# Kernel optimization log

Measured on AMD Instinct MI355X. Metric: run time of the kernel, lower is better.

## Reference

```python
import jax, jax.numpy as jnp
import numpy as np

N = 100000
E = 1600000
IN_DIM = 128
HID = 16      # per-head dim
HEADS = 4
FEAT = HID * HEADS  # 64
OUT_DIM = 64
EPS = 0.5
LAYERS = 2


def setup_inputs() -> dict:
    key = jax.random.key(0)
    ks = jax.random.split(key, 8)
    return {
        "h": jax.random.normal(ks[0], (N, IN_DIM), dtype=jnp.float32),
        "src": jax.random.randint(ks[1], (E,), 0, N, dtype=jnp.int64),
        "dst": jax.random.randint(ks[2], (E,), 0, N, dtype=jnp.int64),
        "t1_W": jax.random.normal(ks[3], (IN_DIM, FEAT), dtype=jnp.float32) * 0.1,
        "t1_b": jnp.zeros((FEAT,), dtype=jnp.float32),
        "t2_W": jax.random.normal(ks[4], (FEAT, OUT_DIM), dtype=jnp.float32) * 0.1,
        "t2_b": jnp.zeros((OUT_DIM,), dtype=jnp.float32),
        "gate_W": jax.random.normal(ks[5], (LAYERS, 2 * HID, 1), dtype=jnp.float32) * 0.2,
        "gate_b": jnp.zeros((LAYERS, 1), dtype=jnp.float32),
    }


def reference(h, src, dst, t1_W, t1_b, t2_W, t2_b, gate_W, gate_b):
    # t1 + relu
    x = jax.nn.relu(h @ t1_W + t1_b)            # [N, FEAT]
    raw = x

    # symmetric degree norm: deg^-0.5 from in-degrees (clamped at 1)
    deg = jax.ops.segment_sum(jnp.ones((E,), x.dtype), dst, num_segments=N)
    norm = jnp.clip(deg, 1.0, None) ** -0.5     # [N]

    xh = x.reshape(N, HEADS, HID)
    edge_norm = norm[dst] * norm[src]           # [E]
    h1 = raw
    # NOTE: original forward never updates x inside the loop; each layer
    # consumes the same relu(t1(h)) and only the last layer's h0 survives.
    for l in range(LAYERS):
        hs = xh[src]                            # [E, H, D] gather src
        hd = xh[dst]                            # [E, H, D] gather dst
        hcat = jnp.concatenate([hd, hs], axis=-1)  # [E, H, 2D]
        s = jnp.tanh(hcat @ gate_W[l] + gate_b[l])[..., 0]  # [E, H]
        s = s * edge_norm[:, None]
        e_h = (hs * s[..., None]).reshape(E, FEAT)          # [E, FEAT]
        h0 = jax.ops.segment_sum(e_h, dst, num_segments=N)  # scatter-sum
        h1 = EPS * raw + h0

    return h1 @ t2_W + t2_b                      # [N, OUT_DIM]
```

## Files before the change

### kernel.cpp

```cpp
#include <hip/hip_runtime.h>
#include <hip/hip_fp16.h>
#include <math.h>

#define N_NODES 100000
#define E_EDGES 1600000
#define IN_DIM  128
#define FEAT    64
#define OUT_DIM 64
#define NBKT    391
#define CAP     6144
#define RNG     4096
#define NSCB    ((E_EDGES + RNG - 1) / RNG)
#define G1B2    ((N_NODES + 127) / 128)
#define HTS     130

typedef float vfloat2 __attribute__((ext_vector_type(2)));

__global__ __launch_bounds__(256) void k_binscatter(
    const int* __restrict__ src, const int* __restrict__ dst,
    int* __restrict__ bucket_cursor, int* __restrict__ binned)
{
    __shared__ int hist[NBKT];
    __shared__ int baseS[NBKT];
    __shared__ int cursor[NBKT];
    __shared__ int gbase[NBKT];
    __shared__ int sA[512], sB[512];
    __shared__ int buf[RNG];
    __shared__ unsigned short bkt[RNG];

    const int tid  = threadIdx.x;
    const int e0   = blockIdx.x * RNG;
    const int ecnt = min(RNG, E_EDGES - e0);

    for (int i = tid; i < NBKT; i += 256) hist[i] = 0;
    __syncthreads();

    int dsave[16];
#pragma unroll
    for (int k = 0; k < 16; ++k) {
        int e = e0 + k * 256 + tid;
        int d = (e < E_EDGES) ? dst[e] : -1;
        dsave[k] = d;
        if (d >= 0) atomicAdd(&hist[d >> 8], 1);
    }
    __syncthreads();

    for (int i = tid; i < 512; i += 256) sA[i] = (i < NBKT) ? hist[i] : 0;
    __syncthreads();
    int* pa = sA; int* pb = sB;
    for (int off = 1; off < 512; off <<= 1) {
        for (int i = tid; i < 512; i += 256)
            pb[i] = pa[i] + ((i >= off) ? pa[i - off] : 0);
        __syncthreads();
        int* t = pa; pa = pb; pb = t;
    }
    for (int i = tid; i < NBKT; i += 256) {
        int ex = pa[i] - hist[i];
        baseS[i]  = ex;
        cursor[i] = ex;
    }
    __syncthreads();

#pragma unroll
    for (int k = 0; k < 16; ++k) {
        int d = dsave[k];
        if (d >= 0) {
            int e   = e0 + k * 256 + tid;
            int s   = src[e];
            int b   = d >> 8;
            int pos = atomicAdd(&cursor[b], 1);
            buf[pos] = ((d & 255) << 17) | s;
            bkt[pos] = (unsigned short)b;
        }
    }
    __syncthreads();

    for (int t = tid; t < NBKT; t += 256) {
        int cnt = hist[t];
        int g   = cnt ? atomicAdd(&bucket_cursor[t], cnt) : 0;
        gbase[t] = g - baseS[t];
    }
    __syncthreads();

    for (int i = tid; i < ecnt; i += 256) {
        int b   = bkt[i];
        int off = gbase[b] + i;
        if (off < CAP) binned[b * CAP + off] = buf[i];
    }
}

__global__ __launch_bounds__(256) void k_bucketfinal(
    const int* __restrict__ binned, const int* __restrict__ bucket_cursor,
    int* __restrict__ deg, int* __restrict__ rowptr, int* __restrict__ src_sorted)
{
    __shared__ int sA[512], sB[512];
    __shared__ int hist[256];
    __shared__ int scn[256];
    __shared__ int cur[256];
    const int b   = blockIdx.x;
    const int tid = threadIdx.x;

    for (int i = tid; i < 512; i += 256) sA[i] = (i < NBKT) ? bucket_cursor[i] : 0;
    __syncthreads();
    int* pa = sA; int* pb = sB;
    for (int off = 1; off < 512; off <<= 1) {
        for (int i = tid; i < 512; i += 256)
            pb[i] = pa[i] + ((i >= off) ? pa[i - off] : 0);
        __syncthreads();
        int* t = pa; pa = pb; pb = t;
    }
    const int cnt  = bucket_cursor[b];
    const int eb   = pa[b] - cnt;
    const int base = b * CAP;
    __syncthreads();

    hist[tid] = 0;
    __syncthreads();
    for (int i = tid; i < cnt; i += 256)
        atomicAdd(&hist[binned[base + i] >> 17], 1);
    __syncthreads();

    int v = hist[tid];
    scn[tid] = v;
    __syncthreads();
    for (int off = 1; off < 256; off <<= 1) {
        int add = (tid >= off) ? scn[tid - off] : 0;
        __syncthreads();
        scn[tid] += add;
        __syncthreads();
    }
    int ex = scn[tid] - v;
    cur[tid] = ex;
    int n = b * 256 + tid;
    if (n < N_NODES) {
        deg[n]    = v;
        rowptr[n] = eb + ex;
    }
    if (b == 0 && tid == 0) rowptr[N_NODES] = E_EDGES;
    __syncthreads();

    for (int i = tid; i < cnt; i += 256) {
        int p   = binned[base + i];
        int dl  = p >> 17;
        int pos = atomicAdd(&cur[dl], 1);
        src_sorted[eb + pos] = p & 0x1FFFF;
    }
}

__global__ __launch_bounds__(256, 3) void k_gemm1(
    const float* __restrict__ h, const float* __restrict__ W1,
    const float* __restrict__ b1, const int* __restrict__ deg,
    const float* __restrict__ gate_W,
    __half* __restrict__ xs2h, unsigned int* __restrict__ xq,
    float* __restrict__ aproj, float* __restrict__ bproj)
{
    __shared__ float Ws[IN_DIM * FEAT];
    __shared__ float hT[16 * HTS];
    const int tid = threadIdx.x;
    const int r0  = blockIdx.x * 128;

    for (int i = tid; i < IN_DIM * FEAT / 4; i += 256)
        ((float4*)Ws)[i] = ((const float4*)W1)[i];

    const int rg = tid >> 2;
    const int cg = tid & 3;
    const int c0 = cg * 16;
    float acc[2][16];
#pragma unroll
    for (int i = 0; i < 2; ++i)
#pragma unroll
        for (int j = 0; j < 16; ++j) acc[i][j] = 0.f;

    for (int kc = 0; kc < IN_DIM / 16; ++kc) {
        float4 f[2];
#pragma unroll
        for (int it = 0; it < 2; ++it) {
            int idx = tid + it * 256;
            int row = idx >> 2;
            int q   = idx & 3;
            int gr  = r0 + row;
            f[it] = (gr < N_NODES)
                ? *(const float4*)(h + (size_t)gr * IN_DIM + kc * 16 + q * 4)
                : make_float4(0.f, 0.f, 0.f, 0.f);
        }
        __syncthreads();
#pragma unroll
        for (int it = 0; it < 2; ++it) {
            int idx = tid + it * 256;
            int row = idx >> 2;
            int q   = idx & 3;
            hT[(q * 4 + 0) * HTS + row] = f[it].x;
            hT[(q * 4 + 1) * HTS + row] = f[it].y;
            hT[(q * 4 + 2) * HTS + row] = f[it].z;
            hT[(q * 4 + 3) * HTS + row] = f[it].w;
        }
        __syncthreads();
#pragma unroll
        for (int kk = 0; kk < 16; ++kk) {
            float2 a2 = *(const float2*)&hT[kk * HTS + rg * 2];
            const float* wrow = &Ws[(kc * 16 + kk) * FEAT + c0];
            float4 w0 = ((const float4*)wrow)[0];
            float4 w1 = ((const float4*)wrow)[1];
            float4 w2 = ((const float4*)wrow)[2];
            float4 w3 = ((const float4*)wrow)[3];
            const float w[16] = {w0.x, w0.y, w0.z, w0.w, w1.x, w1.y, w1.z, w1.w,
                                 w2.x, w2.y, w2.z, w2.w, w3.x, w3.y, w3.z, w3.w};
#pragma unroll
            for (int j = 0; j < 16; ++j) {
                acc[0][j] = fmaf(a2.x, w[j], acc[0][j]);
                acc[1][j] = fmaf(a2.y, w[j], acc[1][j]);
            }
        }
    }

#pragma unroll
    for (int i = 0; i < 2; ++i) {
        int r = r0 + rg * 2 + i;
        if (r >= N_NODES) continue;
        float nr = rsqrtf(fmaxf((float)deg[r], 1.f));
        float xa = 0.f, xb = 0.f;
        alignas(16) __half hv[16];
        float vs[16];
#pragma unroll
        for (int j = 0; j < 16; ++j) {
            float v = acc[i][j] + b1[c0 + j];
            v = v > 0.f ? v : 0.f;
            xa = fmaf(v, gate_W[32 + j], xa);
            xb = fmaf(v, gate_W[48 + j], xb);
            float sv = v * nr;
            vs[j] = sv;
            hv[j] = __float2half(sv);
        }
        float4* xp = (float4*)(xs2h + (size_t)r * FEAT + c0);
        xp[0] = *(const float4*)&hv[0];
        xp[1] = *(const float4*)&hv[8];
        unsigned int u[4];
#pragma unroll
        for (int q = 0; q < 4; ++q) {
            unsigned int t = 0;
            t = __builtin_amdgcn_cvt_pk_fp8_f32(vs[q*4+0], vs[q*4+1], t, false);
            t = __builtin_amdgcn_cvt_pk_fp8_f32(vs[q*4+2], vs[q*4+3], t, true);
            u[q] = t;
        }
        ((uint4*)xq)[(size_t)r * 4 + cg] = make_uint4(u[0], u[1], u[2], u[3]);
        aproj[(size_t)r * 4 + cg] = xa;
        bproj[(size_t)r * 4 + cg] = xb;
    }
}

__global__ __launch_bounds__(256) void k_aggregate(
    const uint4* __restrict__ xq4, const __half2* __restrict__ xs2h2,
    const float* __restrict__ aproj, const float* __restrict__ bproj,
    const int* __restrict__ rowptr, const int* __restrict__ src_sorted,
    const float* __restrict__ gate_b, float* __restrict__ v_out)
{
    const int tid    = threadIdx.x;
    const int lane   = tid & 63;
    const int e      = lane >> 2;
    const int l4     = lane & 3;
    const int wave   = blockIdx.x * 4 + (tid >> 6);
    const int nwaves = gridDim.x * 4;
    const float gb   = gate_b[1];
    const float C    = 2.8853900817779268f;

    for (int n = wave; n < N_NODES; n += nwaves) {
        const int beg = rowptr[n];
        const int end = rowptr[n + 1];
        const int cnt = end - beg;
        const float a_d = aproj[(size_t)n * 4 + l4] + gb;

        float acc[16];
#pragma unroll
        for (int k = 0; k < 16; ++k) acc[k] = 0.f;

        if (cnt > 0) {
            const int last = end - 1;
            int  j0  = beg + e;
            bool ok0 = j0 < end;
            int  s0  = src_sorted[ok0 ? j0 : last];
            uint4 x0 = xq4[(size_t)s0 * 4 + l4];
            float b0 = bproj[(size_t)s0 * 4 + l4];
            int  j1  = j0 + 16;
            bool ok1 = j1 < end;
            int  s1  = src_sorted[ok1 ? j1 : last];

            for (int j = beg; j < end; j += 16) {
                const bool more = (j + 16) < end;
                uint4 x1 = make_uint4(0u, 0u, 0u, 0u);
                float b1 = 0.f;
                int   s2 = s1;
                bool  ok2 = false;
                if (more) {
                    x1 = xq4[(size_t)s1 * 4 + l4];
                    b1 = bproj[(size_t)s1 * 4 + l4];
                    int j2 = j + 32 + e;
                    ok2 = j2 < end;
                    s2 = src_sorted[ok2 ? j2 : last];
                }
                float ex = __builtin_amdgcn_exp2f(C * (a_d + b0));
                float t  = 1.f - 2.f * __builtin_amdgcn_rcpf(ex + 1.f);
                t = ok0 ? t : 0.f;
#pragma unroll
                for (int w = 0; w < 4; ++w) {
                    const unsigned int xw = ((const unsigned int*)&x0)[w];
                    vfloat2 lo = __builtin_amdgcn_cvt_pk_f32_fp8(xw, false);
                    vfloat2 hi = __builtin_amdgcn_cvt_pk_f32_fp8(xw, true);
                    acc[w * 4 + 0] = fmaf(t, lo[0], acc[w * 4 + 0]);
                    acc[w * 4 + 1] = fmaf(t, lo[1], acc[w * 4 + 1]);
                    acc[w * 4 + 2] = fmaf(t, hi[0], acc[w * 4 + 2]);
                    acc[w * 4 + 3] = fmaf(t, hi[1], acc[w * 4 + 3]);
                }
                if (more) {
                    x0 = x1; b0 = b1; ok0 = ok1; ok1 = ok2; s1 = s2;
                }
            }
        }

        const bool elo = (e & 1) == 0;
        float r8[8];
#pragma unroll
        for (int i = 0; i < 8; ++i) {
            float give = elo ? acc[8 + i] : acc[i];
            float got  = __shfl_xor(give, 4, 64);
            r8[i] = (elo ? acc[i] : acc[8 + i]) + got;
        }
        const bool e2lo = (e & 2) == 0;
        float v4[4];
#pragma unroll
        for (int i = 0; i < 4; ++i) {
            float give = e2lo ? r8[4 + i] : r8[i];
            float got  = __shfl_xor(give, 8, 64);
            v4[i] = (e2lo ? r8[i] : r8[4 + i]) + got;
        }
#pragma unroll
        for (int i = 0; i < 4; ++i) v4[i] += __shfl_xor(v4[i], 16, 64);
#pragma unroll
        for (int i = 0; i < 4; ++i) v4[i] += __shfl_xor(v4[i], 32, 64);

        const float dg = fmaxf((float)cnt, 1.f);
        const float nd = rsqrtf(dg);
        const float sd = dg * nd;

        if (e < 4) {
            const int q = ((e & 1) << 1) | ((e >> 1) & 1);
            const int Q = l4 * 4 + q;
            const __half2* hp = xs2h2 + (size_t)n * 32 + Q * 2;
            float2 fa = __half22float2(hp[0]);
            float2 fb = __half22float2(hp[1]);
            float4 v;
            v.x = fmaf(0.5f * sd, fa.x, v4[0] * nd);
            v.y = fmaf(0.5f * sd, fa.y, v4[1] * nd);
            v.z = fmaf(0.5f * sd, fb.x, v4[2] * nd);
            v.w = fmaf(0.5f * sd, fb.y, v4[3] * nd);
            ((float4*)v_out)[(size_t)n * 16 + Q] = v;
        }
    }
}

__global__ __launch_bounds__(256) void k_gemm2(
    float* __restrict__ v, const float* __restrict__ W2, const float* __restrict__ b2)
{
    const int tid    = threadIdx.x;
    const int lane   = tid & 63;
    const int kc     = lane >> 4;
    const int oq     = lane & 15;
    const int wave   = blockIdx.x * 4 + (tid >> 6);
    const int nwaves = gridDim.x * 4;

    float4 wreg[16];
#pragma unroll
    for (int j = 0; j < 16; ++j)
        wreg[j] = *(const float4*)(W2 + (size_t)(kc * 16 + j) * OUT_DIM + oq * 4);
    const float4 bq = ((const float4*)b2)[oq];

    for (int n = wave; n < N_NODES; n += nwaves) {
        const float4* vrow = (const float4*)(v + (size_t)n * FEAT) + kc * 4;
        float4 q0 = vrow[0], q1 = vrow[1], q2 = vrow[2], q3 = vrow[3];
        const float vs[16] = {q0.x, q0.y, q0.z, q0.w, q1.x, q1.y, q1.z, q1.w,
                              q2.x, q2.y, q2.z, q2.w, q3.x, q3.y, q3.z, q3.w};
        float ax = 0.f, ay = 0.f, az = 0.f, aw = 0.f;
#pragma unroll
        for (int j = 0; j < 16; ++j) {
            ax = fmaf(vs[j], wreg[j].x, ax);
            ay = fmaf(vs[j], wreg[j].y, ay);
            az = fmaf(vs[j], wreg[j].z, az);
            aw = fmaf(vs[j], wreg[j].w, aw);
        }
        ax += __shfl_xor(ax, 16, 64); ay += __shfl_xor(ay, 16, 64);
        az += __shfl_xor(az, 16, 64); aw += __shfl_xor(aw, 16, 64);
        ax += __shfl_xor(ax, 32, 64); ay += __shfl_xor(ay, 32, 64);
        az += __shfl_xor(az, 32, 64); aw += __shfl_xor(aw, 32, 64);
        if (kc == 0) {
            float4 o = make_float4(ax + bq.x, ay + bq.y, az + bq.z, aw + bq.w);
            ((float4*)v)[(size_t)n * 16 + oq] = o;
        }
    }
}

extern "C" void kernel_launch(void* const* d_in, const int* in_sizes, int n_in,
                              void* d_out, int out_size, void* d_ws, size_t ws_size,
                              hipStream_t stream)
{
    const float* h   = (const float*)d_in[0];
    const int*   src = (const int*)d_in[1];
    const int*   dst = (const int*)d_in[2];
    const float* W1  = (const float*)d_in[3];
    const float* b1  = (const float*)d_in[4];
    const float* W2  = (const float*)d_in[5];
    const float* b2  = (const float*)d_in[6];
    const float* gW  = (const float*)d_in[7];
    const float* gb  = (const float*)d_in[8];
    float* out = (float*)d_out;

    int* bucket_cursor = (int*)d_ws;
    int* binned        = bucket_cursor + NBKT;
    int* src_sorted    = binned + (size_t)NBKT * CAP;
    int* rowptr        = src_sorted + E_EDGES;
    int* deg           = rowptr + (N_NODES + 1);
    float* aproj       = (float*)(deg + N_NODES);
    float* bproj       = aproj + (size_t)N_NODES * 4;
    __half* xs2h       = (__half*)(bproj + (size_t)N_NODES * 4);
    unsigned int* xq   = (unsigned int*)(xs2h + (size_t)N_NODES * FEAT);

    hipMemsetAsync(bucket_cursor, 0, NBKT * sizeof(int), stream);

    k_binscatter <<<NSCB, 256, 0, stream>>>(src, dst, bucket_cursor, binned);
    k_bucketfinal<<<NBKT, 256, 0, stream>>>(binned, bucket_cursor, deg, rowptr, src_sorted);
    k_gemm1      <<<G1B2, 256, 0, stream>>>(h, W1, b1, deg, gW, xs2h, xq, aproj, bproj);
    k_aggregate  <<<2048, 256, 0, stream>>>((const uint4*)xq, (const __half2*)xs2h,
                                            aproj, bproj, rowptr, src_sorted, gb, out);
    k_gemm2      <<<1024, 256, 0, stream>>>(out, W2, b2);
}
```

Measured before the change: 259.5 us.

## Use 256-row 512-thread blocks in gemm1 with register prefetch of next K-chunk

Each k_gemm1 block now covers 256 rows with 512 threads, so the 32KB W1 copy in shared memory is loaded half as often per row. The next 16-wide slice of h is prefetched into registers while the current slice is being multiplied, overlapping global loads with FMA work. The cost is larger blocks with less control over occupancy, since the min-blocks launch bound was dropped. Shared memory per block also grows with the wider transposed tile.

After: 308.1 us. +18.7%, slower.

```diff
diff --git a/kernel.cpp b/kernel.cpp
--- a/kernel.cpp
+++ b/kernel.cpp
@@ -11,8 +11,7 @@
 #define CAP     6144
 #define RNG     4096
 #define NSCB    ((E_EDGES + RNG - 1) / RNG)
-#define G1B2    ((N_NODES + 127) / 128)
-#define HTS     130
+#define G1B     ((N_NODES + 255) / 256)
 
 typedef float vfloat2 __attribute__((ext_vector_type(2)));
 
@@ -147,7 +146,7 @@
     }
 }
 
-__global__ __launch_bounds__(256, 3) void k_gemm1(
+__global__ __launch_bounds__(512) void k_gemm1(
     const float* __restrict__ h, const float* __restrict__ W1,
     const float* __restrict__ b1, const int* __restrict__ deg,
     const float* __restrict__ gate_W,
@@ -155,11 +154,11 @@
     float* __restrict__ aproj, float* __restrict__ bproj)
 {
     __shared__ float Ws[IN_DIM * FEAT];
-    __shared__ float hT[16 * HTS];
+    __shared__ float hT[16 * 260];
     const int tid = threadIdx.x;
-    const int r0  = blockIdx.x * 128;
-
-    for (int i = tid; i < IN_DIM * FEAT / 4; i += 256)
+    const int r0  = blockIdx.x * 256;
+
+    for (int i = tid; i < IN_DIM * FEAT / 4; i += 512)
         ((float4*)Ws)[i] = ((const float4*)W1)[i];
 
     const int rg = tid >> 2;
@@ -171,33 +170,37 @@
 #pragma unroll
         for (int j = 0; j < 16; ++j) acc[i][j] = 0.f;
 
+    const int qk    = tid & 3;
+    const int row0  = (tid >> 2);
+    const int grow0 = r0 + row0;
+    const int grow1 = r0 + row0 + 128;
+    const bool ok0r = grow0 < N_NODES;
+    const bool ok1r = grow1 < N_NODES;
+    const float* hp0 = h + (size_t)grow0 * IN_DIM + qk * 4;
+    const float* hp1 = h + (size_t)grow1 * IN_DIM + qk * 4;
+
+    float4 f[2];
+    f[0] = ok0r ? *(const float4*)hp0 : make_float4(0.f, 0.f, 0.f, 0.f);
+    f[1] = ok1r ? *(const float4*)hp1 : make_float4(0.f, 0.f, 0.f, 0.f);
+
     for (int kc = 0; kc < IN_DIM / 16; ++kc) {
-        float4 f[2];
+        __syncthreads();
 #pragma unroll
         for (int it = 0; it < 2; ++it) {
-            int idx = tid + it * 256;
-            int row = idx >> 2;
-            int q   = idx & 3;
-            int gr  = r0 + row;
-            f[it] = (gr < N_NODES)
-                ? *(const float4*)(h + (size_t)gr * IN_DIM + kc * 16 + q * 4)
-                : make_float4(0.f, 0.f, 0.f, 0.f);
-        }
-        __syncthreads();
-#pragma unroll
-        for (int it = 0; it < 2; ++it) {
-            int idx = tid + it * 256;
-            int row = idx >> 2;
-            int q   = idx & 3;
-            hT[(q * 4 + 0) * HTS + row] = f[it].x;
-            hT[(q * 4 + 1) * HTS + row] = f[it].y;
-            hT[(q * 4 + 2) * HTS + row] = f[it].z;
-            hT[(q * 4 + 3) * HTS + row] = f[it].w;
-        }
-        __syncthreads();
+            int row = row0 + it * 128;
+            hT[(qk * 4 + 0) * 260 + row] = f[it].x;
+            hT[(qk * 4 + 1) * 260 + row] = f[it].y;
+            hT[(qk * 4 + 2) * 260 + row] = f[it].z;
+            hT[(qk * 4 + 3) * 260 + row] = f[it].w;
+        }
+        __syncthreads();
+        if (kc + 1 < IN_DIM / 16) {
+            if (ok0r) f[0] = *(const float4*)(hp0 + (kc + 1) * 16);
+            if (ok1r) f[1] = *(const float4*)(hp1 + (kc + 1) * 16);
+        }
 #pragma unroll
         for (int kk = 0; kk < 16; ++kk) {
-            float2 a2 = *(const float2*)&hT[kk * HTS + rg * 2];
+            float2 a2 = *(const float2*)&hT[kk * 260 + rg * 2];
             const float* wrow = &Ws[(kc * 16 + kk) * FEAT + c0];
             float4 w0 = ((const float4*)wrow)[0];
             float4 w1 = ((const float4*)wrow)[1];
@@ -426,7 +429,7 @@
 
     k_binscatter <<<NSCB, 256, 0, stream>>>(src, dst, bucket_cursor, binned);
     k_bucketfinal<<<NBKT, 256, 0, stream>>>(binned, bucket_cursor, deg, rowptr, src_sorted);
-    k_gemm1      <<<G1B2, 256, 0, stream>>>(h, W1, b1, deg, gW, xs2h, xq, aproj, bproj);
+    k_gemm1      <<<G1B, 512, 0, stream>>>(h, W1, b1, deg, gW, xs2h, xq, aproj, bproj);
     k_aggregate  <<<2048, 256, 0, stream>>>((const uint4*)xq, (const __half2*)xs2h,
                                             aproj, bproj, rowptr, src_sorted, gb, out);
     k_gemm2      <<<1024, 256, 0, stream>>>(out, W2, b2);
```
